# Optimization experiments

Hardware: AMD Instinct MI355X
Metric: run time of the kernel (lower is better)

## Reference

```python
import jax, jax.numpy as jnp
import numpy as np

BS, G, L, D = 64, 64, 100, 64


def setup_inputs() -> dict:
    key = jax.random.key(0)
    ks = jax.random.split(key, 12)
    s = 1.0 / np.sqrt(D)
    return {
        "seqs": jax.random.normal(ks[0], (BS, G, L, D), dtype=jnp.float32),
        "lens": jax.random.randint(ks[1], (BS, G, 1), 1, L + 1, dtype=jnp.int32),
        "W1": jax.random.normal(ks[2], (D, D), dtype=jnp.float32) * s,
        "W2": jax.random.normal(ks[3], (D, D), dtype=jnp.float32) * s,
        "W3": jax.random.normal(ks[4], (D, D), dtype=jnp.float32) * s,
        "b": jnp.zeros((D,), dtype=jnp.float32),
        "p": jax.random.normal(ks[5], (D,), dtype=jnp.float32) * s,
        "Wq": jax.random.normal(ks[6], (D, 2 * D), dtype=jnp.float32) * s,
        "Wl_0": jax.random.normal(ks[7], (2 * D, 2 * D), dtype=jnp.float32) * s,
        "bl_0": jnp.zeros((2 * D,), dtype=jnp.float32),
        "Wl_1": jax.random.normal(ks[8], (2 * D, 2 * D), dtype=jnp.float32) * s,
        "bl_1": jnp.zeros((2 * D,), dtype=jnp.float32),
    }


def reference(seqs, lens, W1, W2, W3, b, p, Wq, Wl_0, bl_0, Wl_1, bl_1):
    # seqs: [bs, g, L, d]; lens: [bs, g, 1]
    V_last = jnp.einsum('bgd,de->bge', seqs[:, :, -1, :], W1)[:, :, None, :]
    V_seq = jnp.einsum('bgld,de->bgle', seqs, W2)
    avg = jnp.sum(seqs, axis=-2) / lens.astype(jnp.float32)  # [bs, g, d]
    V_avg = jnp.einsum('bgd,de->bge', avg, W3)[:, :, None, :]
    emb = jnp.einsum('bgld,d->bgl', V_last + V_seq + V_avg + b, p)  # [bs, g, L]
    attn = jax.nn.softmax(emb, axis=-1)
    weighted = jnp.einsum('bgl,bgld->bgd', attn, seqs)  # attention-weighted pooling
    h0 = weighted @ Wq  # [bs, g, 2d]
    h = jax.nn.relu(h0 @ Wl_0 + bl_0)
    h = jax.nn.relu(h @ Wl_1 + bl_1)
    return h0 + h  # residual
```

## Files before the change

kernel.cpp:

```cpp
#include <hip/hip_runtime.h>
#include <cstddef>

#define LL 100
#define DD 64
#define NG 4

template<int CTRL>
__device__ __forceinline__ float dpp_add(float x) {
    int s = __builtin_amdgcn_update_dpp(0, __float_as_int(x), CTRL, 0xF, 0xF, true);
    return x + __int_as_float(s);
}

__device__ __forceinline__ float sum16_all(float x) {
    x = dpp_add<0xB1>(x);
    x = dpp_add<0x4E>(x);
    x = dpp_add<0x141>(x);
    x = dpp_add<0x140>(x);
    return x;
}

__global__ __launch_bounds__(256, 4) void seq_encoder_fused(
    const float* __restrict__ seqs,
    const float* __restrict__ W2,  const float* __restrict__ p,
    const float* __restrict__ Wq,  const float* __restrict__ Wl0,
    const float* __restrict__ bl0, const float* __restrict__ Wl1,
    const float* __restrict__ bl1, float* __restrict__ out)
{
    __shared__ __align__(16) float s_q2[DD];
    __shared__ __align__(16) float s_w[NG][DD];
    __shared__ __align__(16) float s_h0[NG][2 * DD];
    __shared__ __align__(16) float s_h1[NG][2 * DD];

    const int tid = threadIdx.x;
    const int r = tid >> 6;
    const int lane = tid & 63;

    {
        const int row = tid >> 2, part = tid & 3;
        const float* wrow = W2 + row * DD + part * 16;
        const float* pp = p + part * 16;
        float s = 0.f;
        #pragma unroll
        for (int e = 0; e < 16; ++e) s += wrow[e] * pp[e];
        s += __shfl_down(s, 2);
        s += __shfl_down(s, 1);
        if (part == 0) s_q2[row] = s;
    }
    __syncthreads();

    const int rg = lane >> 4;
    const int cb = lane & 15;
    const float4 q2v = *(const float4*)&s_q2[cb * 4];

    const int gi = blockIdx.x * NG + r;
    const float4* Sp = (const float4*)(seqs + (size_t)gi * (LL * DD)) + (rg * 16 + cb);

    float z = 0.f;
    float wx = 0.f, wy = 0.f, wz = 0.f, ww = 0.f;

    #pragma unroll
    for (int it = 0; it < LL / 4; ++it) {
        float4 x = Sp[it * 64];
        float t = x.x * q2v.x + x.y * q2v.y + x.z * q2v.z + x.w * q2v.w;
        t = sum16_all(t);
        float e = __expf(t);
        z += e;
        wx += e * x.x;
        wy += e * x.y;
        wz += e * x.z;
        ww += e * x.w;
    }

    z  += __shfl_xor(z, 16);  z  += __shfl_xor(z, 32);
    wx += __shfl_xor(wx, 16); wx += __shfl_xor(wx, 32);
    wy += __shfl_xor(wy, 16); wy += __shfl_xor(wy, 32);
    wz += __shfl_xor(wz, 16); wz += __shfl_xor(wz, 32);
    ww += __shfl_xor(ww, 16); ww += __shfl_xor(ww, 32);

    const float invz = 1.f / z;
    if (rg == 0) {
        float4 o;
        o.x = wx * invz; o.y = wy * invz; o.z = wz * invz; o.w = ww * invz;
        *(float4*)&s_w[r][cb * 4] = o;
    }
    __syncthreads();

    const int jt = tid & 127;
    const int i0 = (tid >> 7) * 2;
    const float4* wva = (const float4*)s_w[i0];
    const float4* wvb = (const float4*)s_w[i0 + 1];
    float h0a = 0.f, h0b = 0.f;
    for (int k4 = 0; k4 < DD / 4; ++k4) {
        float4 xa = wva[k4], xb = wvb[k4];
        const float* wq = Wq + (k4 * 4) * (2 * DD) + jt;
        #pragma unroll
        for (int u = 0; u < 4; ++u) {
            float wv = wq[u * (2 * DD)];
            float av = (&xa.x)[u], bv = (&xb.x)[u];
            h0a += av * wv;
            h0b += bv * wv;
        }
    }
    s_h0[i0][jt] = h0a;
    s_h0[i0 + 1][jt] = h0b;
    __syncthreads();

    float a1m = bl0[jt], b1m = bl0[jt];
    {
        const float4* ha = (const float4*)s_h0[i0];
        const float4* hb = (const float4*)s_h0[i0 + 1];
        for (int k4 = 0; k4 < (2 * DD) / 4; ++k4) {
            float4 xa = ha[k4], xb = hb[k4];
            const float* wl = Wl0 + (k4 * 4) * (2 * DD) + jt;
            #pragma unroll
            for (int u = 0; u < 4; ++u) {
                float wv = wl[u * (2 * DD)];
                a1m += (&xa.x)[u] * wv;
                b1m += (&xb.x)[u] * wv;
            }
        }
    }
    a1m = fmaxf(a1m, 0.f); b1m = fmaxf(b1m, 0.f);
    s_h1[i0][jt] = a1m;
    s_h1[i0 + 1][jt] = b1m;
    __syncthreads();

    float a2m = bl1[jt], b2m = bl1[jt];
    {
        const float4* ha = (const float4*)s_h1[i0];
        const float4* hb = (const float4*)s_h1[i0 + 1];
        for (int k4 = 0; k4 < (2 * DD) / 4; ++k4) {
            float4 xa = ha[k4], xb = hb[k4];
            const float* wl = Wl1 + (k4 * 4) * (2 * DD) + jt;
            #pragma unroll
            for (int u = 0; u < 4; ++u) {
                float wv = wl[u * (2 * DD)];
                a2m += (&xa.x)[u] * wv;
                b2m += (&xb.x)[u] * wv;
            }
        }
    }
    a2m = fmaxf(a2m, 0.f); b2m = fmaxf(b2m, 0.f);

    const size_t gbase = (size_t)blockIdx.x * NG;
    out[(gbase + i0) * (2 * DD) + jt]     = h0a + a2m;
    out[(gbase + i0 + 1) * (2 * DD) + jt] = h0b + b2m;
}

extern "C" void kernel_launch(void* const* d_in, const int* in_sizes, int n_in,
                              void* d_out, int out_size, void* d_ws, size_t ws_size,
                              hipStream_t stream) {
    const float* seqs = (const float*)d_in[0];
    const float* W2   = (const float*)d_in[3];
    const float* p    = (const float*)d_in[6];
    const float* Wq   = (const float*)d_in[7];
    const float* Wl0  = (const float*)d_in[8];
    const float* bl0  = (const float*)d_in[9];
    const float* Wl1  = (const float*)d_in[10];
    const float* bl1  = (const float*)d_in[11];
    float* out = (float*)d_out;

    const int n_groups = 64 * 64;
    seq_encoder_fused<<<n_groups / NG, 256, 0, stream>>>(
        seqs, W2, p, Wq, Wl0, bl0, Wl1, bl1, out);
}
```

Before: 182.1 us.

## Double-buffer sequence loads and split MLP matmuls over K across half-blocks

The streaming softmax-pooling loop now loads sequence rows in batches of five float4s into a two-stage register buffer, so the next batch's loads are issued before the current batch is processed. The three small matmuls are restructured so each thread computes all four groups over half of the K dimension. Partial sums go to a new shared buffer and are combined after a barrier. This cuts per-thread weight loads from global memory by reusing each weight across four groups, at the cost of extra barriers, extra shared memory, and higher register pressure from the load buffers.

```diff
diff --git a/kernel.cpp b/kernel.cpp
--- a/kernel.cpp
+++ b/kernel.cpp
@@ -28,6 +28,7 @@
 {
     __shared__ __align__(16) float s_q2[DD];
     __shared__ __align__(16) float s_w[NG][DD];
+    __shared__ __align__(16) float s_p[2][NG][2 * DD];
     __shared__ __align__(16) float s_h0[NG][2 * DD];
     __shared__ __align__(16) float s_h1[NG][2 * DD];
 
@@ -58,17 +59,28 @@
     float z = 0.f;
     float wx = 0.f, wy = 0.f, wz = 0.f, ww = 0.f;
 
+    float4 buf[2][5];
     #pragma unroll
-    for (int it = 0; it < LL / 4; ++it) {
-        float4 x = Sp[it * 64];
-        float t = x.x * q2v.x + x.y * q2v.y + x.z * q2v.z + x.w * q2v.w;
-        t = sum16_all(t);
-        float e = __expf(t);
-        z += e;
-        wx += e * x.x;
-        wy += e * x.y;
-        wz += e * x.z;
-        ww += e * x.w;
+    for (int j = 0; j < 5; ++j) buf[0][j] = Sp[j * 64];
+    #pragma unroll
+    for (int b = 0; b < 5; ++b) {
+        if (b < 4) {
+            #pragma unroll
+            for (int j = 0; j < 5; ++j)
+                buf[(b + 1) & 1][j] = Sp[((b + 1) * 5 + j) * 64];
+        }
+        #pragma unroll
+        for (int j = 0; j < 5; ++j) {
+            float4 x = buf[b & 1][j];
+            float t = x.x * q2v.x + x.y * q2v.y + x.z * q2v.z + x.w * q2v.w;
+            t = sum16_all(t);
+            float e = __expf(t);
+            z += e;
+            wx += e * x.x;
+            wy += e * x.y;
+            wz += e * x.z;
+            ww += e * x.w;
+        }
     }
 
     z  += __shfl_xor(z, 16);  z  += __shfl_xor(z, 32);
@@ -86,65 +98,76 @@
     __syncthreads();
 
     const int jt = tid & 127;
-    const int i0 = (tid >> 7) * 2;
-    const float4* wva = (const float4*)s_w[i0];
-    const float4* wvb = (const float4*)s_w[i0 + 1];
-    float h0a = 0.f, h0b = 0.f;
-    for (int k4 = 0; k4 < DD / 4; ++k4) {
-        float4 xa = wva[k4], xb = wvb[k4];
-        const float* wq = Wq + (k4 * 4) * (2 * DD) + jt;
-        #pragma unroll
-        for (int u = 0; u < 4; ++u) {
-            float wv = wq[u * (2 * DD)];
-            float av = (&xa.x)[u], bv = (&xb.x)[u];
-            h0a += av * wv;
-            h0b += bv * wv;
+    const int hf = tid >> 7;
+    const int g0 = 2 * hf;
+
+    {
+        float p0 = 0.f, p1 = 0.f, p2 = 0.f, p3 = 0.f;
+        const int k0 = hf * 32;
+        for (int k = k0; k < k0 + 32; ++k) {
+            float wv = Wq[k * (2 * DD) + jt];
+            p0 += s_w[0][k] * wv;
+            p1 += s_w[1][k] * wv;
+            p2 += s_w[2][k] * wv;
+            p3 += s_w[3][k] * wv;
         }
+        s_p[hf][0][jt] = p0; s_p[hf][1][jt] = p1;
+        s_p[hf][2][jt] = p2; s_p[hf][3][jt] = p3;
     }
-    s_h0[i0][jt] = h0a;
-    s_h0[i0 + 1][jt] = h0b;
+    __syncthreads();
+    {
+        float ha = s_p[0][g0][jt] + s_p[1][g0][jt];
+        float hb = s_p[0][g0 + 1][jt] + s_p[1][g0 + 1][jt];
+        s_h0[g0][jt] = ha;
+        s_h0[g0 + 1][jt] = hb;
+    }
     __syncthreads();
 
-    float a1m = bl0[jt], b1m = bl0[jt];
     {
-        const float4* ha = (const float4*)s_h0[i0];
-        const float4* hb = (const float4*)s_h0[i0 + 1];
-        for (int k4 = 0; k4 < (2 * DD) / 4; ++k4) {
-            float4 xa = ha[k4], xb = hb[k4];
-            const float* wl = Wl0 + (k4 * 4) * (2 * DD) + jt;
-            #pragma unroll
-            for (int u = 0; u < 4; ++u) {
-                float wv = wl[u * (2 * DD)];
-                a1m += (&xa.x)[u] * wv;
-                b1m += (&xb.x)[u] * wv;
-            }
+        float p0 = 0.f, p1 = 0.f, p2 = 0.f, p3 = 0.f;
+        const int k0 = hf * 64;
+        for (int k = k0; k < k0 + 64; ++k) {
+            float wv = Wl0[k * (2 * DD) + jt];
+            p0 += s_h0[0][k] * wv;
+            p1 += s_h0[1][k] * wv;
+            p2 += s_h0[2][k] * wv;
+            p3 += s_h0[3][k] * wv;
         }
+        s_p[hf][0][jt] = p0; s_p[hf][1][jt] = p1;
+        s_p[hf][2][jt] = p2; s_p[hf][3][jt] = p3;
     }
-    a1m = fmaxf(a1m, 0.f); b1m = fmaxf(b1m, 0.f);
-    s_h1[i0][jt] = a1m;
-    s_h1[i0 + 1][jt] = b1m;
+    __syncthreads();
+    {
+        float bv = bl0[jt];
+        float ha = fmaxf(s_p[0][g0][jt] + s_p[1][g0][jt] + bv, 0.f);
+        float hb = fmaxf(s_p[0][g0 + 1][jt] + s_p[1][g0 + 1][jt] + bv, 0.f);
+        s_h1[g0][jt] = ha;
+        s_h1[g0 + 1][jt] = hb;
+    }
     __syncthreads();
 
-    float a2m = bl1[jt], b2m = bl1[jt];
     {
-        const float4* ha = (const float4*)s_h1[i0];
-        const float4* hb = (const float4*)s_h1[i0 + 1];
-        for (int k4 = 0; k4 < (2 * DD) / 4; ++k4) {
-            float4 xa = ha[k4], xb = hb[k4];
-            const float* wl = Wl1 + (k4 * 4) * (2 * DD) + jt;
-            #pragma unroll
-            for (int u = 0; u < 4; ++u) {
-                float wv = wl[u * (2 * DD)];
-                a2m += (&xa.x)[u] * wv;
-                b2m += (&xb.x)[u] * wv;
-            }
+        float p0 = 0.f, p1 = 0.f, p2 = 0.f, p3 = 0.f;
+        const int k0 = hf * 64;
+        for (int k = k0; k < k0 + 64; ++k) {
+            float wv = Wl1[k * (2 * DD) + jt];
+            p0 += s_h1[0][k] * wv;
+            p1 += s_h1[1][k] * wv;
+            p2 += s_h1[2][k] * wv;
+            p3 += s_h1[3][k] * wv;
         }
+        s_p[hf][0][jt] = p0; s_p[hf][1][jt] = p1;
+        s_p[hf][2][jt] = p2; s_p[hf][3][jt] = p3;
     }
-    a2m = fmaxf(a2m, 0.f); b2m = fmaxf(b2m, 0.f);
-
-    const size_t gbase = (size_t)blockIdx.x * NG;
-    out[(gbase + i0) * (2 * DD) + jt]     = h0a + a2m;
-    out[(gbase + i0 + 1) * (2 * DD) + jt] = h0b + b2m;
+    __syncthreads();
+    {
+        float bv = bl1[jt];
+        float oa = fmaxf(s_p[0][g0][jt] + s_p[1][g0][jt] + bv, 0.f);
+        float ob = fmaxf(s_p[0][g0 + 1][jt] + s_p[1][g0 + 1][jt] + bv, 0.f);
+        const size_t gbase = (size_t)blockIdx.x * NG;
+        out[(gbase + g0) * (2 * DD) + jt]     = s_h0[g0][jt] + oa;
+        out[(gbase + g0 + 1) * (2 * DD) + jt] = s_h0[g0 + 1][jt] + ob;
+    }
 }
 
 extern "C" void kernel_launch(void* const* d_in, const int* in_sizes, int n_in,
```

After: 180.5 us. Within noise of the previous version (-0.9%).
